# Kernel tuning notes

Hardware: AMD Instinct MI355X
Metric: run time of the kernel (lower is better)

## Reference

```python
import jax, jax.numpy as jnp
import numpy as np

D_MODEL = 1024
N_HEADS = 16
D_K = D_MODEL // N_HEADS
MAX_REL = 128
SEQ = 1024
BATCH = 4


def setup_inputs() -> dict:
    key = jax.random.key(0)
    ks = jax.random.split(key, 8)
    x = jax.random.normal(ks[0], (SEQ, BATCH, D_MODEL), dtype=jnp.float32)
    # nn.Linear weights: shape (out, in), applied as x @ W.T
    w_q = jax.random.normal(ks[1], (D_MODEL, D_MODEL), dtype=jnp.float32) * (1.0 / np.sqrt(D_MODEL))
    w_k = jax.random.normal(ks[2], (D_MODEL, D_MODEL), dtype=jnp.float32) * (1.0 / np.sqrt(D_MODEL))
    w_v = jax.random.normal(ks[3], (D_MODEL, D_MODEL), dtype=jnp.float32) * (1.0 / np.sqrt(D_MODEL))
    w_o = jax.random.normal(ks[4], (D_MODEL, D_MODEL), dtype=jnp.float32) * (1.0 / np.sqrt(D_MODEL))
    b_o = jnp.zeros((D_MODEL,), dtype=jnp.float32)
    rel_k = jax.random.normal(ks[5], (2 * MAX_REL + 1, D_K), dtype=jnp.float32)
    rel_v = jax.random.normal(ks[6], (2 * MAX_REL + 1, D_K), dtype=jnp.float32)
    return {"x": x, "w_q": w_q, "w_k": w_k, "w_v": w_v, "w_o": w_o, "b_o": b_o,
            "rel_k": rel_k, "rel_v": rel_v}


def _relative_positions(seq_len: int) -> jnp.ndarray:
    pos = jnp.arange(seq_len)
    rel = pos[:, None] - pos[None, :]
    rel = jnp.clip(rel, -MAX_REL, MAX_REL) + MAX_REL
    return rel  # [s, t] int indices into relative tables


def reference(x, w_q, w_k, w_v, w_o, b_o, rel_k, rel_v):
    seq_len, batch, _ = x.shape
    scale = 1.0 / np.sqrt(D_K)
    Q = (x @ w_q.T).reshape(seq_len, batch, N_HEADS, D_K)
    K = (x @ w_k.T).reshape(seq_len, batch, N_HEADS, D_K)
    V = (x @ w_v.T).reshape(seq_len, batch, N_HEADS, D_K)

    rel_idx = _relative_positions(seq_len)          # [s, t]
    rk = rel_k[rel_idx]                              # [s, t, d_k]
    rv = rel_v[rel_idx]                              # [s, t, d_k]

    scores = jnp.einsum('sbhd,tbhd->sbth', Q, K) * scale
    scores = scores + jnp.einsum('sbhd,std->sbth', Q, rk) * scale
    # NOTE: original torch code softmaxes over dim=-1 of [s,b,t,h], i.e. the
    # head axis; reproduced faithfully here.
    attn = jax.nn.softmax(scores, axis=-1)           # [s, b, t, h]

    out = jnp.einsum('sbth,tbhd->sbhd', attn, V)
    out = out + jnp.einsum('sbth,std->sbhd', attn, rv)
    out = out.reshape(seq_len, batch, D_MODEL)
    return out @ w_o.T + b_o
```

## Files before the change

kernel.cpp:

```cpp
#include <hip/hip_runtime.h>
#include <stdint.h>

#define DI __device__ __forceinline__

typedef __attribute__((ext_vector_type(8))) short bfx8;
typedef __attribute__((ext_vector_type(4))) short bfx4;
typedef __attribute__((ext_vector_type(4))) float f4;

DI unsigned short f2bf(float x){
  unsigned u = __float_as_uint(x);
  u = (u + 0x7FFFu + ((u >> 16) & 1u)) >> 16;
  return (unsigned short)u;
}
DI float bf2f(unsigned short h){ return __uint_as_float(((unsigned)h) << 16); }

DI f4 mfma32(bfx8 a, bfx8 b, f4 c){
  return __builtin_amdgcn_mfma_f32_16x16x32_bf16(a, b, c, 0, 0, 0);
}
#if __has_builtin(__builtin_amdgcn_mfma_f32_16x16x16bf16_1k)
DI f4 mfma16(bfx4 a, bfx4 b, f4 c){
  return __builtin_amdgcn_mfma_f32_16x16x16bf16_1k(a, b, c, 0, 0, 0);
}
#else
DI f4 mfma16(bfx4 a, bfx4 b, f4 c){
  f4 d = c;
  asm volatile("v_mfma_f32_16x16x16_bf16 %0, %1, %2, %0" : "+v"(d) : "v"(a), "v"(b));
  return d;
}
#endif

DI void gload16(const void* g, void* l){
  __builtin_amdgcn_global_load_lds(
      (__attribute__((address_space(1))) void*)g,
      (__attribute__((address_space(3))) void*)l, 16, 0, 0);
}


__global__ void k_cast(const float* __restrict__ src, unsigned short* __restrict__ dst, int n4){
  int i = blockIdx.x*256 + threadIdx.x;
  if (i < n4){
    const float4 v = ((const float4*)src)[i];
    bfx4 o;
    o[0] = (short)f2bf(v.x); o[1] = (short)f2bf(v.y);
    o[2] = (short)f2bf(v.z); o[3] = (short)f2bf(v.w);
    *(bfx4*)(dst + (size_t)i*4) = o;
  }
}

__global__ void k_castw(const float* __restrict__ s0, const float* __restrict__ s1,
                        const float* __restrict__ s2, const float* __restrict__ s3,
                        unsigned short* __restrict__ dst){
  int i = blockIdx.x*256 + threadIdx.x;
  const float* src = (blockIdx.y==0) ? s0 : (blockIdx.y==1) ? s1 : (blockIdx.y==2) ? s2 : s3;
  const float4 v = ((const float4*)src)[i];
  bfx4 o;
  o[0] = (short)f2bf(v.x); o[1] = (short)f2bf(v.y);
  o[2] = (short)f2bf(v.z); o[3] = (short)f2bf(v.w);
  *(bfx4*)(dst + (size_t)blockIdx.y*1048576 + (size_t)i*4) = o;
}

__global__ void k_relprep(const float* __restrict__ rlk, const float* __restrict__ rlv,
                          unsigned short* __restrict__ relk_bf, unsigned short* __restrict__ relvT_bf){
  int i = blockIdx.x*256 + threadIdx.x;
  if (i < 272*64){
    int r = i >> 6, d = i & 63;
    relk_bf[i] = (r < 257) ? f2bf(rlk[r*64 + d]) : (unsigned short)0;
  }
  if (i < 64*288){
    int d = i / 288, r = i % 288;
    relvT_bf[i] = (r < 257) ? f2bf(rlv[(size_t)r*64 + d]) : (unsigned short)0;
  }
}

__global__ __launch_bounds__(256, 3) void k_qkv(
    const unsigned short* __restrict__ xbf, const unsigned short* __restrict__ wqkv,
    unsigned short* __restrict__ Qf, unsigned short* __restrict__ Kf,
    unsigned short* __restrict__ Vf)
{
  __shared__ __align__(16) unsigned short smem[2][8192];
  const int nt = blockIdx.x;
  const int b  = blockIdx.y;
  const int st = blockIdx.z;
  const int w = threadIdx.x >> 6, lane = threadIdx.x & 63;
  const int wr = w >> 1, wc = w & 1;
  const int p = lane & 15, g = lane >> 4;
  const int s0 = st*128;
  const int n0 = nt*128;
  const f4 fz = {0.f,0.f,0.f,0.f};
  f4 acc[4][4];
#pragma unroll
  for (int m=0;m<4;++m)
#pragma unroll
    for (int n=0;n<4;++n) acc[m][n] = fz;

  const int j0 = w*2, j1 = w*2 + 1;
  const unsigned short* gA = xbf  + (size_t)((s0 + p)*4 + b)*1024 + g*8;
  const unsigned short* gB = wqkv + (size_t)(n0 + p)*1024 + g*8;

  {
    unsigned short* d0 = &smem[0][0];
    gload16(gA + (size_t)j0*65536, d0 + j0*512);
    gload16(gA + (size_t)j1*65536, d0 + j1*512);
    gload16(gB + (size_t)j0*16384, d0 + 4096 + j0*512);
    gload16(gB + (size_t)j1*16384, d0 + 4096 + j1*512);
  }

  for (int it=0; it<32; ++it){
    const int cur = it & 1;
    if (it < 31){
      const int kn = (it+1)*32;
      unsigned short* dn = &smem[cur^1][0];
      gload16(gA + (size_t)j0*65536 + kn, dn + j0*512);
      gload16(gA + (size_t)j1*65536 + kn, dn + j1*512);
      gload16(gB + (size_t)j0*16384 + kn, dn + 4096 + j0*512);
      gload16(gB + (size_t)j1*16384 + kn, dn + 4096 + j1*512);
      asm volatile("s_waitcnt vmcnt(4)" ::: "memory");
    } else {
      asm volatile("s_waitcnt vmcnt(0)" ::: "memory");
    }
    __builtin_amdgcn_sched_barrier(0);
    __builtin_amdgcn_s_barrier();
    __builtin_amdgcn_sched_barrier(0);
    {
      const unsigned short* Ab = &smem[cur][0];
      bfx8 af[4], bfr[4];
#pragma unroll
      for (int m=0;m<4;++m) af[m] = *(const bfx8*)(Ab + (wr*4+m)*512 + lane*8);
#pragma unroll
      for (int n=0;n<4;++n) bfr[n] = *(const bfx8*)(Ab + 4096 + (wc*4+n)*512 + lane*8);
#pragma unroll
      for (int m=0;m<4;++m)
#pragma unroll
        for (int n=0;n<4;++n)
          acc[m][n] = mfma32(af[m], bfr[n], acc[m][n]);
    }
    __builtin_amdgcn_sched_barrier(0);
    __builtin_amdgcn_s_barrier();
    __builtin_amdgcn_sched_barrier(0);
  }

  const int n64 = n0 + wc*64;
  const int sec = n64 >> 10;
  const int h = (n64 & 1023) >> 6;
  float* es = (float*)&smem[0][0] + w*1280;

  if (sec < 2){
    const float scl = (sec == 0) ? 0.125f : 1.0f;
    unsigned short* dst = (sec == 0) ? Qf : Kf;
#pragma unroll
    for (int m=0;m<4;++m){
#pragma unroll
      for (int n=0;n<4;++n)
#pragma unroll
        for (int r=0;r<4;++r)
          es[(4*g + r)*80 + 16*n + p] = acc[m][n][r] * scl;
      __syncthreads();
      f4 v0 = *(const f4*)&es[p*80 + 8*g];
      f4 v1 = *(const f4*)&es[p*80 + 8*g + 4];
      f4 v2 = *(const f4*)&es[p*80 + 32 + 8*g];
      f4 v3 = *(const f4*)&es[p*80 + 32 + 8*g + 4];
      bfx8 lo, hi;
#pragma unroll
      for (int j=0;j<4;++j){
        lo[j]   = (short)f2bf(v0[j]);
        lo[j+4] = (short)f2bf(v1[j]);
        hi[j]   = (short)f2bf(v2[j]);
        hi[j+4] = (short)f2bf(v3[j]);
      }
      size_t fb = ((size_t)(b*16 + h)*64 + (st*8 + wr*4 + m))*1024 + (size_t)lane*16;
      *(bfx8*)(dst + fb) = lo;
      *(bfx8*)(dst + fb + 8) = hi;
      __syncthreads();
    }
  } else {
#pragma unroll
    for (int m=0;m<4;++m){
#pragma unroll
      for (int n=0;n<4;++n)
        *(f4*)&es[(16*n + p)*20 + 4*g] = acc[m][n];
      __syncthreads();
      f4 vv0 = *(const f4*)&es[(p)*20 + 4*g];
      f4 vv1 = *(const f4*)&es[(16 + p)*20 + 4*g];
      f4 vv2 = *(const f4*)&es[(32 + p)*20 + 4*g];
      f4 vv3 = *(const f4*)&es[(48 + p)*20 + 4*g];
      bfx8 lo, hi;
#pragma unroll
      for (int j=0;j<4;++j){
        lo[j]   = (short)f2bf(vv0[j]);
        lo[j+4] = (short)f2bf(vv1[j]);
        hi[j]   = (short)f2bf(vv2[j]);
        hi[j+4] = (short)f2bf(vv3[j]);
      }
      size_t fb = ((size_t)(b*16 + h)*64 + (st*8 + wr*4 + m))*1024 + (size_t)lane*16;
      *(bfx8*)(Vf + fb) = lo;
      *(bfx8*)(Vf + fb + 8) = hi;
      __syncthreads();
    }
  }
}

__global__ __launch_bounds__(256) void k_qr(
    const unsigned short* __restrict__ Qf, const unsigned short* __restrict__ relk,
    unsigned short* __restrict__ Qr2)
{
  __shared__ __align__(16) unsigned short sst[16][16][24];
  const int bx = blockIdx.x;
  const int b  = bx & 3;
  const int st = (bx >> 2) & 63;
  const int uh = bx >> 8;
  const int w = threadIdx.x >> 6, lane = threadIdx.x & 63;
  const int p = lane & 15, g = lane >> 4;
  const int s0 = st << 4;
  const f4 fz = {0.f,0.f,0.f,0.f};

  bfx8 a0[4], a1[4];
#pragma unroll
  for (int hh=0; hh<4; ++hh){
    size_t fb = (((size_t)(b*16 + w*4 + hh))*64 + st)*1024 + (size_t)lane*16;
    a0[hh] = *(const bfx8*)(Qf + fb);
    a1[hh] = *(const bfx8*)(Qf + fb + 8);
  }

  const int c0 = uh ? 9 : 0;
  const int c1 = uh ? 17 : 9;
  const int so = threadIdx.x >> 4, uo = threadIdx.x & 15;

  for (int c=c0; c<c1; ++c){
    const int r0 = c << 4;
    bfx8 b0 = *(const bfx8*)(relk + (size_t)(r0 + p)*64 + 8*g);
    bfx8 b1 = *(const bfx8*)(relk + (size_t)(r0 + p)*64 + 32 + 8*g);
#pragma unroll
    for (int hh=0; hh<4; ++hh){
      f4 acc = mfma32(a1[hh], b1, mfma32(a0[hh], b0, fz));
#pragma unroll
      for (int r=0; r<4; ++r)
        sst[4*g + r][p][w*4 + hh] = f2bf(acc[r]);
    }
    __syncthreads();
    bfx8 v0 = *(const bfx8*)&sst[so][uo][0];
    bfx8 v1 = *(const bfx8*)&sst[so][uo][8];
    size_t ga = (((size_t)b*1024 + s0 + so)*272 + r0 + uo)*16;
    *(bfx8*)(Qr2 + ga) = v0;
    *(bfx8*)(Qr2 + ga + 8) = v1;
    __syncthreads();
  }
}

__global__ __launch_bounds__(256, 2) void k_s(
    const unsigned short* __restrict__ Qf, const unsigned short* __restrict__ Kf,
    const unsigned short* __restrict__ Qr2, float* __restrict__ ivf)
{
  const int pbid = blockIdx.x;
  const int b   = pbid & 3;
  const int ttg = (pbid >> 2) & 15;
  const int st  = pbid >> 6;
  const int w = threadIdx.x >> 6, lane = threadIdx.x & 63;
  const int tt = ttg*4 + w;
  const int p = lane & 15, g = lane >> 4;
  const int s0 = st << 4, t0 = tt << 4;
  const int s = s0 + p;
  const f4 fz = {0.f,0.f,0.f,0.f};

  bfx8 rv[4][2];
#pragma unroll
  for (int r=0; r<4; ++r){
    int t = t0 + 4*g + r;
    int u = s - t + 128; u = u < 0 ? 0 : (u > 256 ? 256 : u);
    const unsigned short* q = Qr2 + (((size_t)b*1024 + s)*272 + u)*16;
    rv[r][0] = *(const bfx8*)q;
    rv[r][1] = *(const bfx8*)(q + 8);
  }

  const unsigned short* qbp = Qf + ((size_t)(b*16)*64 + st)*1024 + (size_t)lane*16;
  const unsigned short* kbp = Kf + ((size_t)(b*16)*64 + tt)*1024 + (size_t)lane*16;

  bfx8 qq[16][2], kk[16][2];
#define LOADH(H) { \
    qq[H][0] = *(const bfx8*)(qbp + (size_t)(H)*65536); \
    qq[H][1] = *(const bfx8*)(qbp + (size_t)(H)*65536 + 8); \
    kk[H][0] = *(const bfx8*)(kbp + (size_t)(H)*65536); \
    kk[H][1] = *(const bfx8*)(kbp + (size_t)(H)*65536 + 8); }

  LOADH(0) LOADH(1) LOADH(2) LOADH(3)

  f4 ps = fz;
#pragma unroll
  for (int h=0; h<16; ++h){
    if (h + 4 < 16){
      const int hn = h + 4;
      qq[hn][0] = *(const bfx8*)(qbp + (size_t)hn*65536);
      qq[hn][1] = *(const bfx8*)(qbp + (size_t)hn*65536 + 8);
      kk[hn][0] = *(const bfx8*)(kbp + (size_t)hn*65536);
      kk[hn][1] = *(const bfx8*)(kbp + (size_t)hn*65536 + 8);
    }
    f4 sc = mfma32(kk[h][1], qq[h][1], mfma32(kk[h][0], qq[h][0], fz));
    const int hg = h >> 3, hr = h & 7;
#pragma unroll
    for (int r=0; r<4; ++r)
      ps[r] += __expf(sc[r] + bf2f((unsigned short)rv[r][hg][hr]));
  }
#undef LOADH

  f4 inv;
#pragma unroll
  for (int r=0; r<4; ++r) inv[r] = 1.0f / ps[r];
  *(f4*)(ivf + (((size_t)(b*64 + tt)*64 + st)*64 + lane)*4) = inv;
}

__global__ __launch_bounds__(256, 2) void k_attn(
    const unsigned short* __restrict__ Qf, const unsigned short* __restrict__ Kf,
    const unsigned short* __restrict__ Vf, const unsigned short* __restrict__ Qr2,
    const float* __restrict__ ivf, const unsigned short* __restrict__ relvT,
    const float* __restrict__ relv, unsigned short* __restrict__ out1)
{
  __shared__ __align__(16) unsigned short skew[128*264];
  const int pbid = blockIdx.x;
  const int xcd = pbid & 7;
  const int b = xcd >> 1;
  const int hhalf = (pbid >> 3) & 1;
  const int st = ((pbid >> 4) << 1) | (xcd & 1);
  const int s0 = st << 4;
  const int w = threadIdx.x >> 6;
  const int lane = threadIdx.x & 63;
  const int p = lane & 15, g = lane >> 4;
  const int s = s0 + p;
  const int hl0 = w * 2;
  const int h0 = hhalf*8 + hl0;
  const f4 fz = {0.f,0.f,0.f,0.f};

  {
    unsigned* zp = (unsigned*)skew + w*4224;
    for (int i = lane; i < 4224; i += 64) zp[i] = 0u;
  }

  bfx8 qf[2][2]; float qr0[2], qr1[2];
#pragma unroll
  for (int hh=0; hh<2; ++hh){
    size_t qb = (((size_t)(b*16 + h0 + hh))*64 + st)*1024 + (size_t)lane*16;
    qf[hh][0] = *(const bfx8*)(Qf + qb);
    qf[hh][1] = *(const bfx8*)(Qf + qb + 8);
    qr0[hh] = bf2f(Qr2[(((size_t)b*1024 + s)*272 + 0)*16 + (h0+hh)]);
    qr1[hh] = bf2f(Qr2[(((size_t)b*1024 + s)*272 + 256)*16 + (h0+hh)]);
  }

  f4 o[2][4];
#pragma unroll
  for (int hh=0; hh<2; ++hh)
#pragma unroll
    for (int df=0; df<4; ++df) o[hh][df] = fz;

  float tl0[2] = {0.f,0.f};
  float tl1[2] = {0.f,0.f};

  const int tlo = (st-8 < 0) ? 0 : st-8;
  const int thi = (st+8 > 63) ? 63 : st+8;

  bfx8 kc[2][2]; bfx4 vc[2][4]; unsigned short qc[2][4]; f4 is;
  bfx8 kn[2][2]; bfx4 vn[2][4]; unsigned short qn[2][4]; f4 isn;

#pragma unroll
  for (int hh=0; hh<2; ++hh){
    size_t bh = (size_t)(b*16 + h0 + hh);
    size_t fb = (bh*64 + 0)*1024 + (size_t)lane*16;
    kc[hh][0] = *(const bfx8*)(Kf + fb);
    kc[hh][1] = *(const bfx8*)(Kf + fb + 8);
#pragma unroll
    for (int df=0; df<4; ++df)
      vc[hh][df] = *(const bfx4*)(Vf + fb + df*4);
  }
  if (0 >= tlo){
#pragma unroll
    for (int hh=0; hh<2; ++hh)
#pragma unroll
      for (int r=0; r<4; ++r){
        int t = 4*g + r;
        int u = s - t + 128; u = u < 0 ? 0 : (u > 256 ? 256 : u);
        qc[hh][r] = Qr2[(((size_t)b*1024 + s)*272 + u)*16 + (h0+hh)];
      }
  }
  is = *(const f4*)(ivf + (((size_t)(b*64 + 0)*64 + st)*64 + lane)*4);

  for (int ti = 0; ti < 64; ++ti){
    const int t0 = ti << 4;
    const bool nearT = (ti >= tlo) && (ti <= thi);

    if (ti < 63){
      const int tn = ti + 1;
#pragma unroll
      for (int hh=0; hh<2; ++hh){
        size_t bh = (size_t)(b*16 + h0 + hh);
        size_t fb = (bh*64 + tn)*1024 + (size_t)lane*16;
        kn[hh][0] = *(const bfx8*)(Kf + fb);
        kn[hh][1] = *(const bfx8*)(Kf + fb + 8);
#pragma unroll
        for (int df=0; df<4; ++df)
          vn[hh][df] = *(const bfx4*)(Vf + fb + df*4);
      }
      if (tn >= tlo && tn <= thi){
#pragma unroll
        for (int hh=0; hh<2; ++hh)
#pragma unroll
          for (int r=0; r<4; ++r){
            int t = (tn<<4) + 4*g + r;
            int u = s - t + 128; u = u < 0 ? 0 : (u > 256 ? 256 : u);
            qn[hh][r] = Qr2[(((size_t)b*1024 + s)*272 + u)*16 + (h0+hh)];
          }
      }
      isn = *(const f4*)(ivf + (((size_t)(b*64 + tn)*64 + st)*64 + lane)*4);
    }

    if (nearT){
#pragma unroll
      for (int hh=0; hh<2; ++hh){
        f4 sc = mfma32(kc[hh][1], qf[hh][1], mfma32(kc[hh][0], qf[hh][0], fz));
        f4 at;
#pragma unroll
        for (int r=0; r<4; ++r) at[r] = __expf(sc[r] + bf2f(qc[hh][r])) * is[r];
        const int row = (hl0 + hh)*16 + p;
#pragma unroll
        for (int r=0; r<4; ++r){
          int t = t0 + 4*g + r;
          int u = s - t + 128;
          float a = at[r];
          if (u <= 0) tl0[hh] += a;
          else if (u >= 256) tl1[hh] += a;
          else skew[row*264 + u] = f2bf(a);
        }
        bfx4 pk;
#pragma unroll
        for (int r=0; r<4; ++r) pk[r] = (short)f2bf(at[r]);
#pragma unroll
        for (int df=0; df<4; ++df)
          o[hh][df] = mfma16(vc[hh][df], pk, o[hh][df]);
      }
    } else {
      const bool hiSide = (ti < st);
#pragma unroll
      for (int hh=0; hh<2; ++hh){
        f4 sc = mfma32(kc[hh][1], qf[hh][1], mfma32(kc[hh][0], qf[hh][0], fz));
        const float qa = hiSide ? qr1[hh] : qr0[hh];
        f4 at;
#pragma unroll
        for (int r=0; r<4; ++r) at[r] = __expf(sc[r] + qa) * is[r];
        float tsum = at[0] + at[1] + at[2] + at[3];
        if (hiSide) tl1[hh] += tsum; else tl0[hh] += tsum;
        bfx4 pk;
#pragma unroll
        for (int r=0; r<4; ++r) pk[r] = (short)f2bf(at[r]);
#pragma unroll
        for (int df=0; df<4; ++df)
          o[hh][df] = mfma16(vc[hh][df], pk, o[hh][df]);
      }
    }

    if (ti < 63){
#pragma unroll
      for (int hh=0; hh<2; ++hh){
#pragma unroll
        for (int kf=0; kf<2; ++kf) kc[hh][kf] = kn[hh][kf];
#pragma unroll
        for (int df=0; df<4; ++df) vc[hh][df] = vn[hh][df];
#pragma unroll
        for (int r=0; r<4; ++r) qc[hh][r] = qn[hh][r];
      }
      is = isn;
    }
  }

  __syncthreads();

  f4 acc2[2][4];
#pragma unroll
  for (int hh=0; hh<2; ++hh)
#pragma unroll
    for (int df=0; df<4; ++df) acc2[hh][df] = fz;
#pragma unroll
  for (int k0=0; k0<256; k0+=32){
    bfx8 bb0 = *(const bfx8*)&skew[(hl0*16 + p)*264 + k0 + 8*g];
    bfx8 bb1 = *(const bfx8*)&skew[((hl0+1)*16 + p)*264 + k0 + 8*g];
#pragma unroll
    for (int df=0; df<4; ++df){
      bfx8 a = *(const bfx8*)(relvT + (size_t)(df*16 + p)*288 + k0 + 8*g);
      acc2[0][df] = mfma32(a, bb0, acc2[0][df]);
      acc2[1][df] = mfma32(a, bb1, acc2[1][df]);
    }
  }

  f4 rv0[4], rv1[4];
#pragma unroll
  for (int df=0; df<4; ++df){
    rv0[df] = *(const f4*)(relv + df*16 + 4*g);
    rv1[df] = *(const f4*)(relv + 16384 + df*16 + 4*g);
  }
#pragma unroll
  for (int hh=0; hh<2; ++hh){
    float tv0 = tl0[hh];
    tv0 += __shfl_xor(tv0, 16, 64);
    tv0 += __shfl_xor(tv0, 32, 64);
    float tv1 = tl1[hh];
    tv1 += __shfl_xor(tv1, 16, 64);
    tv1 += __shfl_xor(tv1, 32, 64);
#pragma unroll
    for (int df=0; df<4; ++df)
#pragma unroll
      for (int r=0; r<4; ++r)
        o[hh][df][r] += acc2[hh][df][r] + tv0*rv0[df][r] + tv1*rv1[df][r];
  }

  __syncthreads();

  float* slabBase = (float*)skew;
  float (*tb)[68] = (float(*)[68])(slabBase + w*(16*68));
#pragma unroll
  for (int hh=0; hh<2; ++hh){
#pragma unroll
    for (int df=0; df<4; ++df)
      *(f4*)&tb[p][df*16 + 4*g] = o[hh][df];
    __syncthreads();
    const int srow = lane >> 2, quad = lane & 3;
    f4 r0 = *(const f4*)&tb[srow][quad*16 + 0];
    f4 r1 = *(const f4*)&tb[srow][quad*16 + 4];
    f4 r2 = *(const f4*)&tb[srow][quad*16 + 8];
    f4 r3 = *(const f4*)&tb[srow][quad*16 + 12];
    size_t addr = ((size_t)b*1024 + s0 + srow)*1024 + (h0+hh)*64 + quad*16;
    bfx8 pa, pb;
#pragma unroll
    for (int j=0; j<4; ++j){
      pa[j]   = (short)f2bf(r0[j]);
      pa[j+4] = (short)f2bf(r1[j]);
      pb[j]   = (short)f2bf(r2[j]);
      pb[j+4] = (short)f2bf(r3[j]);
    }
    *(bfx8*)(out1 + addr) = pa;
    *(bfx8*)(out1 + addr + 8) = pb;
    __syncthreads();
  }
}

__global__ __launch_bounds__(256) void k_wo(
    const unsigned short* __restrict__ out1, const unsigned short* __restrict__ wo,
    const float* __restrict__ bo, float* __restrict__ dout)
{
  __shared__ __align__(16) unsigned short smem[2][6144];
  const int nt = blockIdx.x;
  const int mt = blockIdx.y;
  const int w = threadIdx.x >> 6, lane = threadIdx.x & 63;
  const int wr = w >> 1, wc = w & 1;
  const int p = lane & 15, g = lane >> 4;
  const int m0 = mt*64, n0 = nt*128;
  const f4 fz = {0.f,0.f,0.f,0.f};
  f4 acc[2][4];
#pragma unroll
  for (int m=0;m<2;++m)
#pragma unroll
    for (int n=0;n<4;++n) acc[m][n] = fz;

  const int j0 = w*2, j1 = w*2 + 1;
  const unsigned short* gA = out1 + (size_t)(m0 + p)*1024 + g*8;
  const unsigned short* gB = wo   + (size_t)(n0 + p)*1024 + g*8;

  {
    unsigned short* d0 = &smem[0][0];
    gload16(gA + (size_t)w*16384, d0 + w*512);
    gload16(gB + (size_t)j0*16384, d0 + 2048 + j0*512);
    gload16(gB + (size_t)j1*16384, d0 + 2048 + j1*512);
  }

  for (int it=0; it<32; ++it){
    const int cur = it & 1;
    if (it < 31){
      const int kn = (it+1)*32;
      unsigned short* dn = &smem[cur^1][0];
      gload16(gA + (size_t)w*16384 + kn, dn + w*512);
      gload16(gB + (size_t)j0*16384 + kn, dn + 2048 + j0*512);
      gload16(gB + (size_t)j1*16384 + kn, dn + 2048 + j1*512);
      asm volatile("s_waitcnt vmcnt(3)" ::: "memory");
    } else {
      asm volatile("s_waitcnt vmcnt(0)" ::: "memory");
    }
    __builtin_amdgcn_sched_barrier(0);
    __builtin_amdgcn_s_barrier();
    __builtin_amdgcn_sched_barrier(0);
    {
      const unsigned short* Ab = &smem[cur][0];
      bfx8 af[2], bfr[4];
#pragma unroll
      for (int m=0;m<2;++m) af[m] = *(const bfx8*)(Ab + (wr*2+m)*512 + lane*8);
#pragma unroll
      for (int n=0;n<4;++n) bfr[n] = *(const bfx8*)(Ab + 2048 + (wc*4+n)*512 + lane*8);
#pragma unroll
      for (int m=0;m<2;++m)
#pragma unroll
        for (int n=0;n<4;++n)
          acc[m][n] = mfma32(af[m], bfr[n], acc[m][n]);
    }
    __builtin_amdgcn_sched_barrier(0);
    __builtin_amdgcn_s_barrier();
    __builtin_amdgcn_sched_barrier(0);
  }

#pragma unroll
  for (int n=0;n<4;++n){
    const int col = n0 + wc*64 + n*16 + p;
    const float bias = bo[col];
#pragma unroll
    for (int m=0;m<2;++m)
#pragma unroll
      for (int r=0;r<4;++r){
        int row = m0 + wr*32 + m*16 + 4*g + r;
        int bb = row >> 10, s = row & 1023;
        dout[((size_t)s*4 + bb)*1024 + col] = acc[m][n][r] + bias;
      }
  }
}

extern "C" void kernel_launch(void* const* d_in, const int* in_sizes, int n_in,
                              void* d_out, int out_size, void* d_ws, size_t ws_size,
                              hipStream_t stream){
  const float* x   = (const float*)d_in[0];
  const float* wq  = (const float*)d_in[1];
  const float* wk  = (const float*)d_in[2];
  const float* wv  = (const float*)d_in[3];
  const float* wo  = (const float*)d_in[4];
  const float* bo  = (const float*)d_in[5];
  const float* rlk = (const float*)d_in[6];
  const float* rlv = (const float*)d_in[7];
  char* ws = (char*)d_ws;

  unsigned short* x_bf    = (unsigned short*)(ws + 0);
  unsigned short* wq_bf   = (unsigned short*)(ws + 8388608);
  unsigned short* relk_bf = (unsigned short*)(ws + 16777216);
  unsigned short* relvT_bf= (unsigned short*)(ws + 16812032);
  unsigned short* Qf      = (unsigned short*)(ws + 16848896);
  unsigned short* Kf      = (unsigned short*)(ws + 25237504);
  unsigned short* Vf      = (unsigned short*)(ws + 33626112);
  unsigned short* Qr2     = (unsigned short*)(ws + 42014720);
  unsigned short* out1    = (unsigned short*)(ws + 113317888);
  float*          ivf     = (float*)        (ws + 121706496);
  unsigned short* wo_bf   = (unsigned short*)(ws + 14680064);

  k_cast<<<4096, 256, 0, stream>>>(x, x_bf, 1048576);
  k_castw<<<dim3(1024,4), 256, 0, stream>>>(wq, wk, wv, wo, wq_bf);
  k_relprep<<<72, 256, 0, stream>>>(rlk, rlv, relk_bf, relvT_bf);

  k_qkv<<<dim3(24,4,8), 256, 0, stream>>>(x_bf, wq_bf, Qf, Kf, Vf);
  k_qr<<<512, 256, 0, stream>>>(Qf, relk_bf, Qr2);

  k_s   <<<4096, 256, 0, stream>>>(Qf, Kf, Qr2, ivf);
  k_attn<<<512, 256, 0, stream>>>(Qf, Kf, Vf, Qr2, ivf, relvT_bf, rlv, out1);
  k_wo<<<dim3(8,64), 256, 0, stream>>>(out1, wo_bf, bo, (float*)d_out);
}
```

Measured before the change: 226.6 us.

## Stage Q/K tiles through LDS in k_s with double buffering; widen V loads

k_s now runs 512-thread blocks that each cover two s-tiles and four t-tiles. Six waves copy the Q and K head slices into double-buffered LDS with global_load_lds, so each Q and K tile is fetched once per block and shared across waves instead of every wave loading its own into registers. The cost is a workgroup barrier and vmcnt wait on every head iteration, and two of the eight waves never stage anything. In k_attn, V is now loaded as two 16-byte vectors instead of four 8-byte ones, with the halves split out for the 16x16x16 MFMA.

```diff
diff --git a/kernel.cpp b/kernel.cpp
--- a/kernel.cpp
+++ b/kernel.cpp
@@ -28,6 +28,9 @@
   return d;
 }
 #endif
+
+DI bfx4 lo4(bfx8 v){ bfx4 r; r[0]=v[0]; r[1]=v[1]; r[2]=v[2]; r[3]=v[3]; return r; }
+DI bfx4 hi4(bfx8 v){ bfx4 r; r[0]=v[4]; r[1]=v[5]; r[2]=v[6]; r[3]=v[7]; return r; }
 
 DI void gload16(const void* g, void* l){
   __builtin_amdgcn_global_load_lds(
@@ -246,19 +249,23 @@
   }
 }
 
-__global__ __launch_bounds__(256, 2) void k_s(
+__global__ __launch_bounds__(512, 4) void k_s(
     const unsigned short* __restrict__ Qf, const unsigned short* __restrict__ Kf,
     const unsigned short* __restrict__ Qr2, float* __restrict__ ivf)
 {
+  __shared__ __align__(16) unsigned short qs[2][2][1024];
+  __shared__ __align__(16) unsigned short ks[2][4][1024];
   const int pbid = blockIdx.x;
   const int b   = pbid & 3;
   const int ttg = (pbid >> 2) & 15;
-  const int st  = pbid >> 6;
+  const int stg = pbid >> 6;
   const int w = threadIdx.x >> 6, lane = threadIdx.x & 63;
-  const int tt = ttg*4 + w;
+  const int stl = w >> 2, ttl = w & 3;
+  const int st = stg*2 + stl;
+  const int tt = ttg*4 + ttl;
   const int p = lane & 15, g = lane >> 4;
-  const int s0 = st << 4, t0 = tt << 4;
-  const int s = s0 + p;
+  const int s = (st << 4) + p;
+  const int t0 = tt << 4;
   const f4 fz = {0.f,0.f,0.f,0.f};
 
   bfx8 rv[4][2];
@@ -271,35 +278,52 @@
     rv[r][1] = *(const bfx8*)(q + 8);
   }
 
-  const unsigned short* qbp = Qf + ((size_t)(b*16)*64 + st)*1024 + (size_t)lane*16;
-  const unsigned short* kbp = Kf + ((size_t)(b*16)*64 + tt)*1024 + (size_t)lane*16;
-
-  bfx8 qq[16][2], kk[16][2];
-#define LOADH(H) { \
-    qq[H][0] = *(const bfx8*)(qbp + (size_t)(H)*65536); \
-    qq[H][1] = *(const bfx8*)(qbp + (size_t)(H)*65536 + 8); \
-    kk[H][0] = *(const bfx8*)(kbp + (size_t)(H)*65536); \
-    kk[H][1] = *(const bfx8*)(kbp + (size_t)(H)*65536 + 8); }
-
-  LOADH(0) LOADH(1) LOADH(2) LOADH(3)
+  const bool stager = (w <= 1) || (w >= 4);
+  const unsigned short* gsrc =
+      (w <= 1) ? (Qf + ((size_t)(b*16)*64 + (stg*2 + w))*1024)
+               : (Kf + ((size_t)(b*16)*64 + (ttg*4 + (w & 3)))*1024);
+  unsigned short* ldst[2];
+  ldst[0] = (w <= 1) ? &qs[0][w][0] : &ks[0][w & 3][0];
+  ldst[1] = (w <= 1) ? &qs[1][w][0] : &ks[1][w & 3][0];
+
+  if (stager){
+    gload16(gsrc + (size_t)lane*8, ldst[0]);
+    gload16(gsrc + 512 + (size_t)lane*8, ldst[0] + 512);
+    asm volatile("s_waitcnt vmcnt(0)" ::: "memory");
+  }
+  __builtin_amdgcn_sched_barrier(0);
+  __builtin_amdgcn_s_barrier();
+  __builtin_amdgcn_sched_barrier(0);
 
   f4 ps = fz;
 #pragma unroll
   for (int h=0; h<16; ++h){
-    if (h + 4 < 16){
-      const int hn = h + 4;
-      qq[hn][0] = *(const bfx8*)(qbp + (size_t)hn*65536);
-      qq[hn][1] = *(const bfx8*)(qbp + (size_t)hn*65536 + 8);
-      kk[hn][0] = *(const bfx8*)(kbp + (size_t)hn*65536);
-      kk[hn][1] = *(const bfx8*)(kbp + (size_t)hn*65536 + 8);
-    }
-    f4 sc = mfma32(kk[h][1], qq[h][1], mfma32(kk[h][0], qq[h][0], fz));
-    const int hg = h >> 3, hr = h & 7;
-#pragma unroll
-    for (int r=0; r<4; ++r)
-      ps[r] += __expf(sc[r] + bf2f((unsigned short)rv[r][hg][hr]));
-  }
-#undef LOADH
+    const int buf = h & 1;
+    if (h < 15 && stager){
+      unsigned short* ld = ldst[buf ^ 1];
+      gload16(gsrc + (size_t)(h+1)*65536 + (size_t)lane*8, ld);
+      gload16(gsrc + (size_t)(h+1)*65536 + 512 + (size_t)lane*8, ld + 512);
+    }
+    {
+      const unsigned short* qb = &qs[buf][stl][lane*16];
+      const unsigned short* kb = &ks[buf][ttl][lane*16];
+      bfx8 q0 = *(const bfx8*)qb;
+      bfx8 q1 = *(const bfx8*)(qb + 8);
+      bfx8 k0 = *(const bfx8*)kb;
+      bfx8 k1 = *(const bfx8*)(kb + 8);
+      f4 sc = mfma32(k1, q1, mfma32(k0, q0, fz));
+      const int hg = h >> 3, hr = h & 7;
+#pragma unroll
+      for (int r=0; r<4; ++r)
+        ps[r] += __expf(sc[r] + bf2f((unsigned short)rv[r][hg][hr]));
+    }
+    if (h < 15){
+      if (stager) asm volatile("s_waitcnt vmcnt(0)" ::: "memory");
+      __builtin_amdgcn_sched_barrier(0);
+      __builtin_amdgcn_s_barrier();
+      __builtin_amdgcn_sched_barrier(0);
+    }
+  }
 
   f4 inv;
 #pragma unroll
@@ -355,8 +379,8 @@
   const int tlo = (st-8 < 0) ? 0 : st-8;
   const int thi = (st+8 > 63) ? 63 : st+8;
 
-  bfx8 kc[2][2]; bfx4 vc[2][4]; unsigned short qc[2][4]; f4 is;
-  bfx8 kn[2][2]; bfx4 vn[2][4]; unsigned short qn[2][4]; f4 isn;
+  bfx8 kc[2][2]; bfx8 vc8[2][2]; unsigned short qc[2][4]; f4 is;
+  bfx8 kn[2][2]; bfx8 vn8[2][2]; unsigned short qn[2][4]; f4 isn;
 
 #pragma unroll
   for (int hh=0; hh<2; ++hh){
@@ -364,9 +388,8 @@
     size_t fb = (bh*64 + 0)*1024 + (size_t)lane*16;
     kc[hh][0] = *(const bfx8*)(Kf + fb);
     kc[hh][1] = *(const bfx8*)(Kf + fb + 8);
-#pragma unroll
-    for (int df=0; df<4; ++df)
-      vc[hh][df] = *(const bfx4*)(Vf + fb + df*4);
+    vc8[hh][0] = *(const bfx8*)(Vf + fb);
+    vc8[hh][1] = *(const bfx8*)(Vf + fb + 8);
   }
   if (0 >= tlo){
 #pragma unroll
@@ -392,9 +415,8 @@
         size_t fb = (bh*64 + tn)*1024 + (size_t)lane*16;
         kn[hh][0] = *(const bfx8*)(Kf + fb);
         kn[hh][1] = *(const bfx8*)(Kf + fb + 8);
-#pragma unroll
-        for (int df=0; df<4; ++df)
-          vn[hh][df] = *(const bfx4*)(Vf + fb + df*4);
+        vn8[hh][0] = *(const bfx8*)(Vf + fb);
+        vn8[hh][1] = *(const bfx8*)(Vf + fb + 8);
       }
       if (tn >= tlo && tn <= thi){
 #pragma unroll
@@ -429,9 +451,10 @@
         bfx4 pk;
 #pragma unroll
         for (int r=0; r<4; ++r) pk[r] = (short)f2bf(at[r]);
-#pragma unroll
-        for (int df=0; df<4; ++df)
-          o[hh][df] = mfma16(vc[hh][df], pk, o[hh][df]);
+        o[hh][0] = mfma16(lo4(vc8[hh][0]), pk, o[hh][0]);
+        o[hh][1] = mfma16(hi4(vc8[hh][0]), pk, o[hh][1]);
+        o[hh][2] = mfma16(lo4(vc8[hh][1]), pk, o[hh][2]);
+        o[hh][3] = mfma16(hi4(vc8[hh][1]), pk, o[hh][3]);
       }
     } else {
       const bool hiSide = (ti < st);
@@ -447,9 +470,10 @@
         bfx4 pk;
 #pragma unroll
         for (int r=0; r<4; ++r) pk[r] = (short)f2bf(at[r]);
-#pragma unroll
-        for (int df=0; df<4; ++df)
-          o[hh][df] = mfma16(vc[hh][df], pk, o[hh][df]);
+        o[hh][0] = mfma16(lo4(vc8[hh][0]), pk, o[hh][0]);
+        o[hh][1] = mfma16(hi4(vc8[hh][0]), pk, o[hh][1]);
+        o[hh][2] = mfma16(lo4(vc8[hh][1]), pk, o[hh][2]);
+        o[hh][3] = mfma16(hi4(vc8[hh][1]), pk, o[hh][3]);
       }
     }
 
@@ -457,9 +481,7 @@
 #pragma unroll
       for (int hh=0; hh<2; ++hh){
 #pragma unroll
-        for (int kf=0; kf<2; ++kf) kc[hh][kf] = kn[hh][kf];
-#pragma unroll
-        for (int df=0; df<4; ++df) vc[hh][df] = vn[hh][df];
+        for (int kf=0; kf<2; ++kf){ kc[hh][kf] = kn[hh][kf]; vc8[hh][kf] = vn8[hh][kf]; }
 #pragma unroll
         for (int r=0; r<4; ++r) qc[hh][r] = qn[hh][r];
       }
@@ -646,7 +668,7 @@
   k_qkv<<<dim3(24,4,8), 256, 0, stream>>>(x_bf, wq_bf, Qf, Kf, Vf);
   k_qr<<<512, 256, 0, stream>>>(Qf, relk_bf, Qr2);
 
-  k_s   <<<4096, 256, 0, stream>>>(Qf, Kf, Qr2, ivf);
+  k_s   <<<2048, 512, 0, stream>>>(Qf, Kf, Qr2, ivf);
   k_attn<<<512, 256, 0, stream>>>(Qf, Kf, Vf, Qr2, ivf, relvT_bf, rlv, out1);
   k_wo<<<dim3(8,64), 256, 0, stream>>>(out1, wo_bf, bo, (float*)d_out);
 }
```

Result: no change. 223.9 us (-1.2%).
